# Optimization experiments

Hardware: AMD Instinct MI355X
Metric: run time of the kernel (lower is better)

## Reference

```python
import jax, jax.numpy as jnp
import numpy as np

B, C, H, W = 2, 256, 64, 64
NUM_HEADS = 4
DIM_HEAD_QK = 64
DIM_HEAD_V = 64  # dim_out // num_heads
DIM_OUT_QK = NUM_HEADS * DIM_HEAD_QK  # 256
DIM_OUT_V = NUM_HEADS * DIM_HEAD_V    # 256
SCALE = DIM_HEAD_QK ** -0.5


def rel_logits_1d(q, rel_k, permute):
    # q: (Bh, Hq, Wq, d), rel_k: (2*Wq-1, d)
    Bh, Hq, Wq, d = q.shape
    R = 2 * Wq - 1
    x = jnp.einsum('bhwd,rd->bhwr', q, rel_k)              # (Bh, Hq, Wq, R)
    x = x.reshape(-1, Wq, R)
    x_pad = jnp.pad(x, ((0, 0), (0, 0), (0, 1))).reshape(x.shape[0], -1)
    x_pad = jnp.pad(x_pad, ((0, 0), (0, Wq - 1)))
    x_pad = x_pad.reshape(-1, Wq + 1, R)
    x = x_pad[:, :Wq, Wq - 1:]                              # (Bh*Hq, Wq, Wq)
    x = x.reshape(Bh, Hq, 1, Wq, Wq)
    x = jnp.broadcast_to(x, (Bh, Hq, Hq, Wq, Wq))
    return jnp.transpose(x, permute)


def pos_embed_rel(q, height_rel, width_rel):
    # q: (Bh, HW, d)
    Bh = q.shape[0]
    qr = q.reshape(Bh, H, W, -1)
    rel_w = rel_logits_1d(qr, width_rel, (0, 1, 3, 2, 4))   # (Bh, H, W, H, W)
    qt = jnp.transpose(qr, (0, 2, 1, 3))                    # (Bh, W, H, d)
    rel_h = rel_logits_1d(qt, height_rel, (0, 3, 1, 4, 2))  # (Bh, H, W, H, W)
    return (rel_h + rel_w).reshape(Bh, H * W, H * W)


def setup_inputs() -> dict:
    key = jax.random.key(0)
    k1, k2, k3, k4 = jax.random.split(key, 4)
    x = jax.random.normal(k1, (B, C, H, W), dtype=jnp.float32)
    qkv_w = jax.random.normal(k2, (2 * DIM_OUT_QK + DIM_OUT_V, C), dtype=jnp.float32) * (C ** -0.5)
    height_rel = jax.random.normal(k3, (2 * H - 1, DIM_HEAD_QK), dtype=jnp.float32) * SCALE
    width_rel = jax.random.normal(k4, (2 * W - 1, DIM_HEAD_QK), dtype=jnp.float32) * SCALE
    return {"x": x, "qkv_w": qkv_w, "height_rel": height_rel, "width_rel": width_rel}


def reference(x, qkv_w, height_rel, width_rel):
    # 1x1 conv == channel matmul
    qkv = jnp.einsum('bchw,oc->bohw', x, qkv_w)             # (B, 768, H, W)
    q, k, v = jnp.split(qkv, [DIM_OUT_QK, 2 * DIM_OUT_QK], axis=1)
    HW = H * W
    q = q.reshape(B * NUM_HEADS, DIM_HEAD_QK, HW).transpose(0, 2, 1)  # (Bh, HW, d)
    k = k.reshape(B * NUM_HEADS, DIM_HEAD_QK, HW)                     # (Bh, d, HW)
    v = v.reshape(B * NUM_HEADS, DIM_HEAD_V, HW).transpose(0, 2, 1)   # (Bh, HW, dv)
    attn = jnp.einsum('bnd,bdm->bnm', q, k) * SCALE + pos_embed_rel(q, height_rel, width_rel)
    attn = jax.nn.softmax(attn, axis=-1)
    out = jnp.einsum('bnm,bmd->bnd', attn, v)               # (Bh, HW, dv)
    out = out.transpose(0, 2, 1).reshape(B, DIM_OUT_V, H, W)
    return out
```

## Files before the change

kernel.cpp:

```cpp
#include <hip/hip_runtime.h>
#include <hip/hip_bf16.h>

typedef __attribute__((ext_vector_type(8))) short bf16x8;
typedef __attribute__((ext_vector_type(4))) float f32x4;

static __device__ __forceinline__ f32x4 mfma16(bf16x8 a, bf16x8 b, f32x4 c) {
    return __builtin_amdgcn_mfma_f32_16x16x32_bf16(a, b, c, 0, 0, 0);
}
static __device__ __forceinline__ void gll16(const void* g, void* l) {
    __builtin_amdgcn_global_load_lds(
        (const __attribute__((address_space(1))) unsigned int*)g,
        (__attribute__((address_space(3))) unsigned int*)l, 16, 0, 0);
}

#define LOG2E 1.44269504f

__global__ __launch_bounds__(256, 4) void qkv_kernel(
    const float* __restrict__ x, const float* __restrict__ w,
    __hip_bfloat16* __restrict__ qb, __hip_bfloat16* __restrict__ kb,
    __hip_bfloat16* __restrict__ vt)
{
    alignas(16) __shared__ __hip_bfloat16 sA[64 * 72];
    alignas(16) __shared__ __hip_bfloat16 sB[64 * 72];
    const int nb = blockIdx.x * 64;
    const int ob = blockIdx.y * 64;
    const int b  = blockIdx.z;
    const int tid  = threadIdx.x;
    const int lane = tid & 63;
    const int wv   = tid >> 6;
    const int quad = lane >> 4;
    const int l16  = lane & 15;

    f32x4 acc[4];
    for (int i = 0; i < 4; i++) acc[i] = (f32x4)0.f;

    for (int k0 = 0; k0 < 256; k0 += 64) {
        __syncthreads();
        {
            const int o = tid >> 2, c0 = (tid & 3) << 4;
            const float* srcw = w + (ob + o) * 256 + k0 + c0;
            union { bf16x8 v; __hip_bfloat16 h[8]; } u0, u1;
            #pragma unroll
            for (int i = 0; i < 2; i++) {
                float4 f = *(const float4*)(srcw + i * 4);
                u0.h[4*i+0] = __float2bfloat16(f.x); u0.h[4*i+1] = __float2bfloat16(f.y);
                u0.h[4*i+2] = __float2bfloat16(f.z); u0.h[4*i+3] = __float2bfloat16(f.w);
            }
            #pragma unroll
            for (int i = 0; i < 2; i++) {
                float4 f = *(const float4*)(srcw + 8 + i * 4);
                u1.h[4*i+0] = __float2bfloat16(f.x); u1.h[4*i+1] = __float2bfloat16(f.y);
                u1.h[4*i+2] = __float2bfloat16(f.z); u1.h[4*i+3] = __float2bfloat16(f.w);
            }
            *(bf16x8*)&sA[o * 72 + c0]     = u0.v;
            *(bf16x8*)&sA[o * 72 + c0 + 8] = u1.v;
        }
        {
            const int c = tid >> 2, n0 = (tid & 3) << 4;
            const int csw = c ^ ((tid & 3) * 16);
            const float* srcx = x + ((size_t)b * 256 + k0 + c) * 4096 + nb + n0;
            #pragma unroll
            for (int i = 0; i < 4; i++) {
                float4 f = *(const float4*)(srcx + i * 4);
                sB[(n0 + 4*i + 0) * 72 + csw] = __float2bfloat16(f.x);
                sB[(n0 + 4*i + 1) * 72 + csw] = __float2bfloat16(f.y);
                sB[(n0 + 4*i + 2) * 72 + csw] = __float2bfloat16(f.z);
                sB[(n0 + 4*i + 3) * 72 + csw] = __float2bfloat16(f.w);
            }
        }
        __syncthreads();
        const __hip_bfloat16* aRow = &sA[(16 * wv + l16) * 72];
        #pragma unroll
        for (int ks = 0; ks < 2; ks++) {
            bf16x8 af = *(const bf16x8*)&aRow[ks * 32 + quad * 8];
            #pragma unroll
            for (int ct = 0; ct < 4; ct++) {
                bf16x8 bfv = *(const bf16x8*)&sB[(16 * ct + l16) * 72
                                                 + ((ks * 32 + quad * 8) ^ (ct * 16))];
                acc[ct] = mfma16(af, bfv, acc[ct]);
            }
        }
    }
    if (ob < 512) {
        __syncthreads();
        #pragma unroll
        for (int ct = 0; ct < 4; ct++) {
            union { short4 s; __hip_bfloat16 hh[4]; } u;
            #pragma unroll
            for (int r = 0; r < 4; r++) u.hh[r] = __float2bfloat16(acc[ct][r]);
            *(short4*)&sA[(16 * ct + l16) * 72 + 16 * wv + 4 * quad] = u.s;
        }
        __syncthreads();
        const int n_l = tid >> 2, d16 = (tid & 3) * 16;
        const int n = nb + n_l;
        const __hip_bfloat16* srcl = &sA[n_l * 72 + d16];
        bf16x8 v0 = *(const bf16x8*)srcl;
        bf16x8 v1 = *(const bf16x8*)(srcl + 8);
        const int bhh = b * 4 + ((ob & 255) >> 6);
        if (ob < 256) {
            __hip_bfloat16* dst = qb + ((size_t)bhh * 4096 + n) * 64;
            *(bf16x8*)(dst + d16)     = v0;
            *(bf16x8*)(dst + d16 + 8) = v1;
        } else {
            const int s = (n & 7) << 3;
            __hip_bfloat16* dst = kb + ((size_t)bhh * 4096 + n) * 64;
            *(bf16x8*)(dst + (d16 ^ s))       = v0;
            *(bf16x8*)(dst + ((d16 + 8) ^ s)) = v1;
        }
    } else {
        __syncthreads();
        #pragma unroll
        for (int ct = 0; ct < 4; ct++)
            #pragma unroll
            for (int r = 0; r < 4; r++)
                sA[(16 * wv + quad * 4 + r) * 72 + 16 * ct + l16] = __float2bfloat16(acc[ct][r]);
        int o2 = (ob - 512) + 16 * wv + l16;
        int bhh = b * 4 + (o2 >> 6), d = o2 & 63;
        const __hip_bfloat16* srcl = &sA[(16 * wv + l16) * 72 + 16 * quad];
        __hip_bfloat16* vrow = vt + ((size_t)bhh * 64 + d) * 4096;
        const int kt = quad & 1;
        const int gbase = nb + (quad >> 1) * 32;
        const int dsw = (d & 7) << 3;
        #pragma unroll
        for (int m = 0; m < 4; m++) {
            short4 val = *(const short4*)(srcl + 4 * m);
            int P4 = gbase + 8 * m + 4 * kt;
            *(short4*)(vrow + (P4 ^ dsw)) = val;
        }
    }
}

__global__ __launch_bounds__(512, 4) void attn_kernel(
    const __hip_bfloat16* __restrict__ qb, const __hip_bfloat16* __restrict__ kb,
    const __hip_bfloat16* __restrict__ vt, const float* __restrict__ hrel,
    const float* __restrict__ wrel, float* __restrict__ out)
{
    extern __shared__ __align__(16) char smem[];
    alignas(16) __shared__ __hip_bfloat16 sRH[64 * 66];

    const int h    = blockIdx.x;
    const int bh   = blockIdx.y;
    const int tid  = threadIdx.x;
    const int lane = tid & 63;
    const int wv   = tid >> 6;
    const int qg   = wv >> 2;
    const int kg   = wv & 3;
    const int quad = lane >> 4;
    const int l16  = lane & 15;

    __hip_bfloat16* sQ   = (__hip_bfloat16*)smem;
    __hip_bfloat16* sW   = (__hip_bfloat16*)smem + 64 * 72;
    __hip_bfloat16* sHRs = (__hip_bfloat16*)smem + 192 * 72;
    __hip_bfloat16* sRWt = (__hip_bfloat16*)smem;

    {
        int r = tid >> 3, d8 = (tid & 7) * 8;
        *(bf16x8*)&sQ[r * 72 + d8] =
            *(const bf16x8*)&qb[(((size_t)bh * 4096 + h * 64 + r)) * 64 + d8];
    }
    {
        int r = tid >> 2, c0 = (tid & 3) << 4;
        union { bf16x8 v; __hip_bfloat16 h8[8]; } u0, u1;
        #pragma unroll
        for (int i = 0; i < 2; i++) {
            float4 f = (r < 127) ? *(const float4*)&wrel[r * 64 + c0 + 4*i] : float4{0,0,0,0};
            u0.h8[4*i+0] = __float2bfloat16(f.x); u0.h8[4*i+1] = __float2bfloat16(f.y);
            u0.h8[4*i+2] = __float2bfloat16(f.z); u0.h8[4*i+3] = __float2bfloat16(f.w);
        }
        #pragma unroll
        for (int i = 0; i < 2; i++) {
            float4 f = (r < 127) ? *(const float4*)&wrel[r * 64 + c0 + 8 + 4*i] : float4{0,0,0,0};
            u1.h8[4*i+0] = __float2bfloat16(f.x); u1.h8[4*i+1] = __float2bfloat16(f.y);
            u1.h8[4*i+2] = __float2bfloat16(f.z); u1.h8[4*i+3] = __float2bfloat16(f.w);
        }
        *(bf16x8*)&sW[r * 72 + c0]     = u0.v;
        *(bf16x8*)&sW[r * 72 + c0 + 8] = u1.v;
    }
    {
        int r = tid >> 3, c0 = (tid & 7) * 8;
        union { bf16x8 v; __hip_bfloat16 h8[8]; } u0;
        #pragma unroll
        for (int i = 0; i < 2; i++) {
            float4 f = *(const float4*)&hrel[(63 - h + r) * 64 + c0 + 4*i];
            u0.h8[4*i+0] = __float2bfloat16(f.x); u0.h8[4*i+1] = __float2bfloat16(f.y);
            u0.h8[4*i+2] = __float2bfloat16(f.z); u0.h8[4*i+3] = __float2bfloat16(f.w);
        }
        *(bf16x8*)&sHRs[r * 72 + c0] = u0.v;
    }
    __syncthreads();

    const int g    = wv & 3;
    const int half = wv >> 2;
    const __hip_bfloat16* aRow = &sQ[(16 * g + l16) * 72];
    bf16x8 qf0 = *(const bf16x8*)&aRow[quad * 8];
    bf16x8 qf1 = *(const bf16x8*)&aRow[32 + quad * 8];
    bf16x8 qm[2][2];
    #pragma unroll
    for (int qt = 0; qt < 2; qt++) {
        const __hip_bfloat16* qr = &sQ[(qg * 32 + 16 * qt + l16) * 72];
        qm[qt][0] = *(const bf16x8*)&qr[quad * 8];
        qm[qt][1] = *(const bf16x8*)&qr[32 + quad * 8];
    }
    __syncthreads();

    {
        const int rbase = half * 64;
        #pragma unroll
        for (int ct = 0; ct < 4; ct++) {
            int rr = rbase + 16 * ct + l16;
            f32x4 a = (f32x4)0.f;
            a = mfma16(qf0, *(const bf16x8*)&sW[rr * 72 + quad * 8], a);
            a = mfma16(qf1, *(const bf16x8*)&sW[rr * 72 + 32 + quad * 8], a);
            #pragma unroll
            for (int r = 0; r < 4; r++) {
                int ww = 16 * g + quad * 4 + r;
                int wp = rr + ww - 63;
                if (wp >= 0 && wp < 64) sRWt[ww * 68 + wp] = __float2bfloat16(a[r]);
            }
        }
    }
    if (half == 0) {
        #pragma unroll
        for (int ct = 0; ct < 4; ct++) {
            f32x4 a = (f32x4)0.f;
            a = mfma16(qf0, *(const bf16x8*)&sHRs[(16 * ct + l16) * 72 + quad * 8], a);
            a = mfma16(qf1, *(const bf16x8*)&sHRs[(16 * ct + l16) * 72 + 32 + quad * 8], a);
            #pragma unroll
            for (int r = 0; r < 4; r++)
                sRH[(16 * g + quad * 4 + r) * 66 + 16 * ct + l16] = __float2bfloat16(a[r]);
        }
    }
    __syncthreads();

    union S4 { short4 s; __hip_bfloat16 h[4]; };
    float rwf[2][2][4];
    #pragma unroll
    for (int qt = 0; qt < 2; qt++)
        #pragma unroll
        for (int kt = 0; kt < 2; kt++) {
            S4 t;
            t.s = *(const short4*)&sRWt[(qg * 32 + 16 * qt + l16) * 68
                                        + 32 * (kg & 1) + 16 * kt + 4 * quad];
            #pragma unroll
            for (int r = 0; r < 4; r++)
                rwf[qt][kt][r] = LOG2E * __bfloat162float(t.h[r]);
        }
    __syncthreads();

    const char* kT = (const char*)kb + (size_t)bh * 524288 + wv * 1024 + lane * 16;
    const char* vT = (const char*)vt + (size_t)bh * 524288
                     + (size_t)(wv * 4 + quad) * 8192 + l16 * 16;

    gll16(kT,           smem + wv * 1024);
    gll16(kT + 8192,    smem + 8192 + wv * 1024);
    gll16(vT,           smem + 16384 + wv * 1024);
    gll16(vT + 262144,  smem + 24576 + wv * 1024);
    __syncthreads();

    f32x4 oacc[2][4];
    #pragma unroll
    for (int qt = 0; qt < 2; qt++)
        #pragma unroll
        for (int dt = 0; dt < 4; dt++) oacc[qt][dt] = (f32x4)0.f;
    f32x4 lacc[2] = {(f32x4)0.f, (f32x4)0.f};
    const bf16x8 vones = (bf16x8)(short)0x3F80;

    const int krowOff = (kg * 32 + l16) * 128;
    const int sw  = (l16 & 7) << 4;
    const int kA  = (quad * 16) ^ sw;
    const int kB  = (64 + quad * 16) ^ sw;
    const int vOff = 16384 + l16 * 256 + ((kg * 64 + quad * 16) ^ sw);

    const __hip_bfloat16* rh0 = &sRH[(qg * 32 + l16) * 66];
    const __hip_bfloat16* rh1 = &sRH[(qg * 32 + 16 + l16) * 66];
    const float SC = 0.125f * LOG2E;

    for (int j = 0; j < 32; j++) {
        const char* buf = smem + (j & 1) * 32768;
        if (j < 31) {
            char* nbuf = smem + ((j + 1) & 1) * 32768;
            const char* gk = kT + (size_t)(j + 1) * 16384;
            gll16(gk,          nbuf + wv * 1024);
            gll16(gk + 8192,   nbuf + 8192 + wv * 1024);
            const char* gv = vT + (size_t)(j + 1) * 256;
            gll16(gv,          nbuf + 16384 + wv * 1024);
            gll16(gv + 262144, nbuf + 24576 + wv * 1024);
        }

        const char* kr = buf + krowOff;
        bf16x8 kf00 = *(const bf16x8*)(kr + kA);
        bf16x8 kf01 = *(const bf16x8*)(kr + kB);
        bf16x8 kf10 = *(const bf16x8*)(kr + 2048 + kA);
        bf16x8 kf11 = *(const bf16x8*)(kr + 2048 + kB);

        f32x4 s[2][2];
        __builtin_amdgcn_s_setprio(1);
        #pragma unroll
        for (int qt = 0; qt < 2; qt++) {
            f32x4 a0 = (f32x4)0.f, a1 = (f32x4)0.f;
            a0 = mfma16(kf00, qm[qt][0], a0);
            a0 = mfma16(kf01, qm[qt][1], a0);
            a1 = mfma16(kf10, qm[qt][0], a1);
            a1 = mfma16(kf11, qm[qt][1], a1);
            s[qt][0] = a0; s[qt][1] = a1;
        }
        __builtin_amdgcn_s_setprio(0);

        const int hp = 2 * j + (kg >> 1);
        bf16x8 pa[2];
        #pragma unroll
        for (int qt = 0; qt < 2; qt++) {
            float rhb = LOG2E * __bfloat162float((qt ? rh1 : rh0)[hp]);
            float pv[8];
            #pragma unroll
            for (int r = 0; r < 4; r++)
                pv[r] = __builtin_amdgcn_exp2f(fmaf(s[qt][0][r], SC, rwf[qt][0][r] + rhb));
            #pragma unroll
            for (int r = 0; r < 4; r++)
                pv[4 + r] = __builtin_amdgcn_exp2f(fmaf(s[qt][1][r], SC, rwf[qt][1][r] + rhb));
            union { bf16x8 v; __hip_bfloat162 b2[4]; } pu;
            #pragma unroll
            for (int pi = 0; pi < 4; pi++)
                pu.b2[pi] = __float22bfloat162_rn(float2{pv[2 * pi], pv[2 * pi + 1]});
            pa[qt] = pu.v;
        }

        __builtin_amdgcn_s_setprio(1);
        #pragma unroll
        for (int dt = 0; dt < 4; dt++) {
            bf16x8 vf = *(const bf16x8*)(buf + vOff + dt * 4096);
            oacc[0][dt] = mfma16(pa[0], vf, oacc[0][dt]);
            oacc[1][dt] = mfma16(pa[1], vf, oacc[1][dt]);
        }
        lacc[0] = mfma16(pa[0], vones, lacc[0]);
        lacc[1] = mfma16(pa[1], vones, lacc[1]);
        __builtin_amdgcn_s_setprio(0);
        __syncthreads();
    }

    float* obuf = (float*)smem;
    if (kg != 0) {
        float* rb = obuf + (kg - 1) * 4672;
        #pragma unroll
        for (int qt = 0; qt < 2; qt++)
            #pragma unroll
            for (int dt = 0; dt < 4; dt++)
                *(f32x4*)&rb[qg * 2304 + (16 * dt + l16) * 36 + 16 * qt + 4 * quad]
                    = oacc[qt][dt];
        if (l16 == 0)
            #pragma unroll
            for (int qt = 0; qt < 2; qt++)
                #pragma unroll
                for (int r = 0; r < 4; r++)
                    rb[4608 + qg * 32 + 16 * qt + 4 * quad + r] = lacc[qt][r];
    }
    __syncthreads();
    if (kg == 0) {
        #pragma unroll
        for (int rg = 0; rg < 3; rg++) {
            const float* rb = obuf + rg * 4672;
            #pragma unroll
            for (int qt = 0; qt < 2; qt++) {
                #pragma unroll
                for (int dt = 0; dt < 4; dt++)
                    oacc[qt][dt] += *(const f32x4*)&rb[qg * 2304 + (16 * dt + l16) * 36
                                                       + 16 * qt + 4 * quad];
                #pragma unroll
                for (int r = 0; r < 4; r++)
                    lacc[qt][r] += rb[4608 + qg * 32 + 16 * qt + 4 * quad + r];
            }
        }
        const int b = bh >> 2, head = bh & 3;
        #pragma unroll
        for (int qt = 0; qt < 2; qt++) {
            f32x4 lv;
            #pragma unroll
            for (int r = 0; r < 4; r++) lv[r] = 1.f / lacc[qt][r];
            #pragma unroll
            for (int dt = 0; dt < 4; dt++) {
                f32x4 o = oacc[qt][dt] * lv;
                int dv = 16 * dt + l16;
                int q0 = qg * 32 + 16 * qt + 4 * quad;
                *(f32x4*)&out[((size_t)(b * 256 + head * 64 + dv)) * 4096 + h * 64 + q0] = o;
            }
        }
    }
}

extern "C" void kernel_launch(void* const* d_in, const int* in_sizes, int n_in,
                              void* d_out, int out_size, void* d_ws, size_t ws_size,
                              hipStream_t stream) {
    const float* x     = (const float*)d_in[0];
    const float* qkv_w = (const float*)d_in[1];
    const float* hrel  = (const float*)d_in[2];
    const float* wrel  = (const float*)d_in[3];
    float* out = (float*)d_out;

    __hip_bfloat16* qb = (__hip_bfloat16*)d_ws;
    __hip_bfloat16* kb = qb + (size_t)8 * 4096 * 64;
    __hip_bfloat16* vt = kb + (size_t)8 * 4096 * 64;

    qkv_kernel<<<dim3(64, 12, 2), 256, 0, stream>>>(x, qkv_w, qb, kb, vt);
    attn_kernel<<<dim3(64, 8), 512, 65536, stream>>>(qb, kb, vt, hrel, wrel, out);
}
```

Before: 125.4 us.

## Prefetch QKV projection tiles into registers and deepen attention K/V pipeline

In the QKV projection kernel, the next k-slice of weights and inputs is now loaded into registers while the current slice is being multiplied, so global load latency overlaps the MFMAs. In the attention kernel, K/V tiles are issued two iterations ahead into the double buffer. Partial vmcnt waits plus raw s_barrier replace the full __syncthreads, so one tile's loads stay in flight while the other is consumed. This adds register pressure in the projection kernel. It also relies on correct manual waitcnt counting, and the LDS-direct loads must not race with the barriers.

```diff
diff --git a/kernel.cpp b/kernel.cpp
--- a/kernel.cpp
+++ b/kernel.cpp
@@ -34,41 +34,56 @@
     f32x4 acc[4];
     for (int i = 0; i < 4; i++) acc[i] = (f32x4)0.f;
 
-    for (int k0 = 0; k0 < 256; k0 += 64) {
+    const int oA = tid >> 2, cA = (tid & 3) << 4;
+    const float* srcw = w + (ob + oA) * 256 + cA;
+    const int cB = tid >> 2, nB = (tid & 3) << 4;
+    const int csw = cB ^ ((tid & 3) * 16);
+    const float* srcx = x + ((size_t)b * 256 + cB) * 4096 + nb + nB;
+
+    float4 ra[4], rb4[4];
+    #pragma unroll
+    for (int i = 0; i < 4; i++) ra[i]  = *(const float4*)(srcw + i * 4);
+    #pragma unroll
+    for (int i = 0; i < 4; i++) rb4[i] = *(const float4*)(srcx + i * 4);
+
+    for (int t = 0; t < 4; t++) {
         __syncthreads();
         {
-            const int o = tid >> 2, c0 = (tid & 3) << 4;
-            const float* srcw = w + (ob + o) * 256 + k0 + c0;
             union { bf16x8 v; __hip_bfloat16 h[8]; } u0, u1;
             #pragma unroll
             for (int i = 0; i < 2; i++) {
-                float4 f = *(const float4*)(srcw + i * 4);
+                float4 f = ra[i];
                 u0.h[4*i+0] = __float2bfloat16(f.x); u0.h[4*i+1] = __float2bfloat16(f.y);
                 u0.h[4*i+2] = __float2bfloat16(f.z); u0.h[4*i+3] = __float2bfloat16(f.w);
             }
             #pragma unroll
             for (int i = 0; i < 2; i++) {
-                float4 f = *(const float4*)(srcw + 8 + i * 4);
+                float4 f = ra[2 + i];
                 u1.h[4*i+0] = __float2bfloat16(f.x); u1.h[4*i+1] = __float2bfloat16(f.y);
                 u1.h[4*i+2] = __float2bfloat16(f.z); u1.h[4*i+3] = __float2bfloat16(f.w);
             }
-            *(bf16x8*)&sA[o * 72 + c0]     = u0.v;
-            *(bf16x8*)&sA[o * 72 + c0 + 8] = u1.v;
+            *(bf16x8*)&sA[oA * 72 + cA]     = u0.v;
+            *(bf16x8*)&sA[oA * 72 + cA + 8] = u1.v;
         }
         {
-            const int c = tid >> 2, n0 = (tid & 3) << 4;
-            const int csw = c ^ ((tid & 3) * 16);
-            const float* srcx = x + ((size_t)b * 256 + k0 + c) * 4096 + nb + n0;
             #pragma unroll
             for (int i = 0; i < 4; i++) {
-                float4 f = *(const float4*)(srcx + i * 4);
-                sB[(n0 + 4*i + 0) * 72 + csw] = __float2bfloat16(f.x);
-                sB[(n0 + 4*i + 1) * 72 + csw] = __float2bfloat16(f.y);
-                sB[(n0 + 4*i + 2) * 72 + csw] = __float2bfloat16(f.z);
-                sB[(n0 + 4*i + 3) * 72 + csw] = __float2bfloat16(f.w);
+                float4 f = rb4[i];
+                sB[(nB + 4*i + 0) * 72 + csw] = __float2bfloat16(f.x);
+                sB[(nB + 4*i + 1) * 72 + csw] = __float2bfloat16(f.y);
+                sB[(nB + 4*i + 2) * 72 + csw] = __float2bfloat16(f.z);
+                sB[(nB + 4*i + 3) * 72 + csw] = __float2bfloat16(f.w);
             }
         }
         __syncthreads();
+        if (t < 3) {
+            #pragma unroll
+            for (int i = 0; i < 4; i++)
+                ra[i]  = *(const float4*)(srcw + (t + 1) * 64 + i * 4);
+            #pragma unroll
+            for (int i = 0; i < 4; i++)
+                rb4[i] = *(const float4*)(srcx + (size_t)(t + 1) * 64 * 4096 + i * 4);
+        }
         const __hip_bfloat16* aRow = &sA[(16 * wv + l16) * 72];
         #pragma unroll
         for (int ks = 0; ks < 2; ks++) {
@@ -251,11 +266,14 @@
     const char* vT = (const char*)vt + (size_t)bh * 524288
                      + (size_t)(wv * 4 + quad) * 8192 + l16 * 16;
 
-    gll16(kT,           smem + wv * 1024);
-    gll16(kT + 8192,    smem + 8192 + wv * 1024);
-    gll16(vT,           smem + 16384 + wv * 1024);
-    gll16(vT + 262144,  smem + 24576 + wv * 1024);
-    __syncthreads();
+    gll16(kT,                smem + wv * 1024);
+    gll16(kT + 8192,         smem + 8192 + wv * 1024);
+    gll16(vT,                smem + 16384 + wv * 1024);
+    gll16(vT + 262144,       smem + 24576 + wv * 1024);
+    gll16(kT + 16384,        smem + 32768 + wv * 1024);
+    gll16(kT + 16384 + 8192, smem + 32768 + 8192 + wv * 1024);
+    gll16(vT + 256,          smem + 32768 + 16384 + wv * 1024);
+    gll16(vT + 262144 + 256, smem + 32768 + 24576 + wv * 1024);
 
     f32x4 oacc[2][4];
     #pragma unroll
@@ -277,15 +295,10 @@
 
     for (int j = 0; j < 32; j++) {
         const char* buf = smem + (j & 1) * 32768;
-        if (j < 31) {
-            char* nbuf = smem + ((j + 1) & 1) * 32768;
-            const char* gk = kT + (size_t)(j + 1) * 16384;
-            gll16(gk,          nbuf + wv * 1024);
-            gll16(gk + 8192,   nbuf + 8192 + wv * 1024);
-            const char* gv = vT + (size_t)(j + 1) * 256;
-            gll16(gv,          nbuf + 16384 + wv * 1024);
-            gll16(gv + 262144, nbuf + 24576 + wv * 1024);
-        }
+        if (j < 31) asm volatile("s_waitcnt vmcnt(4)" ::: "memory");
+        else        asm volatile("s_waitcnt vmcnt(0)" ::: "memory");
+        __builtin_amdgcn_s_barrier();
+        __builtin_amdgcn_sched_barrier(0);
 
         const char* kr = buf + krowOff;
         bf16x8 kf00 = *(const bf16x8*)(kr + kA);
@@ -335,7 +348,18 @@
         lacc[0] = mfma16(pa[0], vones, lacc[0]);
         lacc[1] = mfma16(pa[1], vones, lacc[1]);
         __builtin_amdgcn_s_setprio(0);
-        __syncthreads();
+
+        __builtin_amdgcn_sched_barrier(0);
+        __builtin_amdgcn_s_barrier();
+        if (j < 30) {
+            char* nb2 = smem + (j & 1) * 32768;
+            const char* gk = kT + (size_t)(j + 2) * 16384;
+            gll16(gk,          nb2 + wv * 1024);
+            gll16(gk + 8192,   nb2 + 8192 + wv * 1024);
+            const char* gv = vT + (size_t)(j + 2) * 256;
+            gll16(gv,          nb2 + 16384 + wv * 1024);
+            gll16(gv + 262144, nb2 + 24576 + wv * 1024);
+        }
     }
 
     float* obuf = (float*)smem;
```

Result: no change. 127.8 us (+1.9%).

## Pre-transpose x to bf16 and double-buffer QKV projection with async LDS loads

Applied to the files above, without the earlier changes.

Adds a prep kernel that converts x to bf16 in a swizzled position-major layout, staged through the output buffer as scratch. The QKV GEMM then streams x tiles into LDS with global_load_lds and double-buffers them. Each wave keeps its weight fragments in registers rather than staging them through shared memory. This removes the per-block redundant fp32 conversion and strided transposed LDS stores. The cost is an extra kernel launch and an extra pass over x through global memory.

```diff
diff --git a/kernel.cpp b/kernel.cpp
--- a/kernel.cpp
+++ b/kernel.cpp
@@ -12,16 +12,57 @@
         (const __attribute__((address_space(1))) unsigned int*)g,
         (__attribute__((address_space(3))) unsigned int*)l, 16, 0, 0);
 }
+static __device__ __forceinline__ bf16x8 pack8(float4 a, float4 b) {
+    union { bf16x8 v; __hip_bfloat162 h[4]; } u;
+    u.h[0] = __float22bfloat162_rn(float2{a.x, a.y});
+    u.h[1] = __float22bfloat162_rn(float2{a.z, a.w});
+    u.h[2] = __float22bfloat162_rn(float2{b.x, b.y});
+    u.h[3] = __float22bfloat162_rn(float2{b.z, b.w});
+    return u.v;
+}
 
 #define LOG2E 1.44269504f
 
+__global__ __launch_bounds__(256, 8) void prep_kernel(
+    const float* __restrict__ x, __hip_bfloat16* __restrict__ xt)
+{
+    alignas(16) __shared__ __hip_bfloat16 sT[64 * 72];
+    const int bx = blockIdx.x;
+    const int by = blockIdx.y;
+    const int b  = blockIdx.z;
+    const int tid = threadIdx.x;
+
+    const int cp = tid >> 3;
+    const int n8 = (tid & 7) * 8;
+    const float* s0 = x + ((size_t)b * 256 + by * 64 + 2 * cp) * 4096 + bx * 64 + n8;
+    float4 f0 = *(const float4*)(s0);
+    float4 f1 = *(const float4*)(s0 + 4);
+    float4 g0 = *(const float4*)(s0 + 4096);
+    float4 g1 = *(const float4*)(s0 + 4096 + 4);
+    float c0v[8] = {f0.x, f0.y, f0.z, f0.w, f1.x, f1.y, f1.z, f1.w};
+    float c1v[8] = {g0.x, g0.y, g0.z, g0.w, g1.x, g1.y, g1.z, g1.w};
+    #pragma unroll
+    for (int i = 0; i < 8; i++) {
+        __hip_bfloat162 p = __float22bfloat162_rn(float2{c0v[i], c1v[i]});
+        *(__hip_bfloat162*)&sT[(n8 + i) * 72 + 2 * cp] = p;
+    }
+    __syncthreads();
+
+    const int n = tid >> 2, c16 = (tid & 3) * 16;
+    bf16x8 v0 = *(const bf16x8*)&sT[n * 72 + c16];
+    bf16x8 v1 = *(const bf16x8*)&sT[n * 72 + c16 + 8];
+    const int s = (n & 7) << 3;
+    __hip_bfloat16* dst = xt + ((size_t)b * 4096 + bx * 64 + n) * 256 + by * 64;
+    *(bf16x8*)(dst + (c16 ^ s))       = v0;
+    *(bf16x8*)(dst + ((c16 + 8) ^ s)) = v1;
+}
+
 __global__ __launch_bounds__(256, 4) void qkv_kernel(
-    const float* __restrict__ x, const float* __restrict__ w,
+    const float* __restrict__ w, const __hip_bfloat16* __restrict__ xt,
     __hip_bfloat16* __restrict__ qb, __hip_bfloat16* __restrict__ kb,
     __hip_bfloat16* __restrict__ vt)
 {
-    alignas(16) __shared__ __hip_bfloat16 sA[64 * 72];
-    alignas(16) __shared__ __hip_bfloat16 sB[64 * 72];
+    extern __shared__ __align__(16) char smem[];
     const int nb = blockIdx.x * 64;
     const int ob = blockIdx.y * 64;
     const int b  = blockIdx.z;
@@ -31,69 +72,63 @@
     const int quad = lane >> 4;
     const int l16  = lane & 15;
 
+    const char* xbase = (const char*)xt
+        + ((size_t)b * 4096 + nb + 16 * wv + (lane >> 3)) * 512 + (lane & 7) * 16;
+
+    gll16(xbase,        smem + wv * 2048);
+    gll16(xbase + 4096, smem + wv * 2048 + 1024);
+
+    bf16x8 af[4][2];
+    {
+        const float* wrow = w + (ob + 16 * wv + l16) * 256 + quad * 8;
+        #pragma unroll
+        for (int t = 0; t < 4; t++)
+            #pragma unroll
+            for (int ks = 0; ks < 2; ks++) {
+                const float* p = wrow + t * 64 + ks * 32;
+                af[t][ks] = pack8(*(const float4*)p, *(const float4*)(p + 4));
+            }
+    }
     f32x4 acc[4];
+    #pragma unroll
     for (int i = 0; i < 4; i++) acc[i] = (f32x4)0.f;
 
-    for (int k0 = 0; k0 < 256; k0 += 64) {
+    __syncthreads();
+
+    const int swB = (l16 & 7) << 4;
+    #pragma unroll
+    for (int t = 0; t < 4; t++) {
+        if (t < 3) {
+            char* nbuf = smem + ((t + 1) & 1) * 8192;
+            gll16(xbase + (t + 1) * 128,        nbuf + wv * 2048);
+            gll16(xbase + (t + 1) * 128 + 4096, nbuf + wv * 2048 + 1024);
+        }
+        const char* buf = smem + (t & 1) * 8192;
+        #pragma unroll
+        for (int ks = 0; ks < 2; ks++) {
+            #pragma unroll
+            for (int ct = 0; ct < 4; ct++) {
+                bf16x8 bfv = *(const bf16x8*)(buf + (16 * ct + l16) * 128
+                                              + ((ks * 64 + quad * 16) ^ swB));
+                acc[ct] = mfma16(af[t][ks], bfv, acc[ct]);
+            }
+        }
         __syncthreads();
-        {
-            const int o = tid >> 2, c0 = (tid & 3) << 4;
-            const float* srcw = w + (ob + o) * 256 + k0 + c0;
-            union { bf16x8 v; __hip_bfloat16 h[8]; } u0, u1;
-            #pragma unroll
-            for (int i = 0; i < 2; i++) {
-                float4 f = *(const float4*)(srcw + i * 4);
-                u0.h[4*i+0] = __float2bfloat16(f.x); u0.h[4*i+1] = __float2bfloat16(f.y);
-                u0.h[4*i+2] = __float2bfloat16(f.z); u0.h[4*i+3] = __float2bfloat16(f.w);
-            }
-            #pragma unroll
-            for (int i = 0; i < 2; i++) {
-                float4 f = *(const float4*)(srcw + 8 + i * 4);
-                u1.h[4*i+0] = __float2bfloat16(f.x); u1.h[4*i+1] = __float2bfloat16(f.y);
-                u1.h[4*i+2] = __float2bfloat16(f.z); u1.h[4*i+3] = __float2bfloat16(f.w);
-            }
-            *(bf16x8*)&sA[o * 72 + c0]     = u0.v;
-            *(bf16x8*)&sA[o * 72 + c0 + 8] = u1.v;
-        }
-        {
-            const int c = tid >> 2, n0 = (tid & 3) << 4;
-            const int csw = c ^ ((tid & 3) * 16);
-            const float* srcx = x + ((size_t)b * 256 + k0 + c) * 4096 + nb + n0;
-            #pragma unroll
-            for (int i = 0; i < 4; i++) {
-                float4 f = *(const float4*)(srcx + i * 4);
-                sB[(n0 + 4*i + 0) * 72 + csw] = __float2bfloat16(f.x);
-                sB[(n0 + 4*i + 1) * 72 + csw] = __float2bfloat16(f.y);
-                sB[(n0 + 4*i + 2) * 72 + csw] = __float2bfloat16(f.z);
-                sB[(n0 + 4*i + 3) * 72 + csw] = __float2bfloat16(f.w);
-            }
-        }
-        __syncthreads();
-        const __hip_bfloat16* aRow = &sA[(16 * wv + l16) * 72];
-        #pragma unroll
-        for (int ks = 0; ks < 2; ks++) {
-            bf16x8 af = *(const bf16x8*)&aRow[ks * 32 + quad * 8];
-            #pragma unroll
-            for (int ct = 0; ct < 4; ct++) {
-                bf16x8 bfv = *(const bf16x8*)&sB[(16 * ct + l16) * 72
-                                                 + ((ks * 32 + quad * 8) ^ (ct * 16))];
-                acc[ct] = mfma16(af, bfv, acc[ct]);
-            }
-        }
-    }
+    }
+
+    __hip_bfloat16* eA = (__hip_bfloat16*)smem;
     if (ob < 512) {
-        __syncthreads();
         #pragma unroll
         for (int ct = 0; ct < 4; ct++) {
             union { short4 s; __hip_bfloat16 hh[4]; } u;
             #pragma unroll
             for (int r = 0; r < 4; r++) u.hh[r] = __float2bfloat16(acc[ct][r]);
-            *(short4*)&sA[(16 * ct + l16) * 72 + 16 * wv + 4 * quad] = u.s;
+            *(short4*)&eA[(16 * ct + l16) * 72 + 16 * wv + 4 * quad] = u.s;
         }
         __syncthreads();
         const int n_l = tid >> 2, d16 = (tid & 3) * 16;
         const int n = nb + n_l;
-        const __hip_bfloat16* srcl = &sA[n_l * 72 + d16];
+        const __hip_bfloat16* srcl = &eA[n_l * 72 + d16];
         bf16x8 v0 = *(const bf16x8*)srcl;
         bf16x8 v1 = *(const bf16x8*)(srcl + 8);
         const int bhh = b * 4 + ((ob & 255) >> 6);
@@ -108,15 +143,14 @@
             *(bf16x8*)(dst + ((d16 + 8) ^ s)) = v1;
         }
     } else {
-        __syncthreads();
         #pragma unroll
         for (int ct = 0; ct < 4; ct++)
             #pragma unroll
             for (int r = 0; r < 4; r++)
-                sA[(16 * wv + quad * 4 + r) * 72 + 16 * ct + l16] = __float2bfloat16(acc[ct][r]);
+                eA[(16 * wv + quad * 4 + r) * 72 + 16 * ct + l16] = __float2bfloat16(acc[ct][r]);
         int o2 = (ob - 512) + 16 * wv + l16;
         int bhh = b * 4 + (o2 >> 6), d = o2 & 63;
-        const __hip_bfloat16* srcl = &sA[(16 * wv + l16) * 72 + 16 * quad];
+        const __hip_bfloat16* srcl = &eA[(16 * wv + l16) * 72 + 16 * quad];
         __hip_bfloat16* vrow = vt + ((size_t)bhh * 64 + d) * 4096;
         const int kt = quad & 1;
         const int gbase = nb + (quad >> 1) * 32;
@@ -399,7 +433,9 @@
     __hip_bfloat16* qb = (__hip_bfloat16*)d_ws;
     __hip_bfloat16* kb = qb + (size_t)8 * 4096 * 64;
     __hip_bfloat16* vt = kb + (size_t)8 * 4096 * 64;
-
-    qkv_kernel<<<dim3(64, 12, 2), 256, 0, stream>>>(x, qkv_w, qb, kb, vt);
+    __hip_bfloat16* xt = (__hip_bfloat16*)d_out;
+
+    prep_kernel<<<dim3(64, 4, 2), 256, 0, stream>>>(x, xt);
+    qkv_kernel<<<dim3(64, 12, 2), 256, 16384, stream>>>(qkv_w, xt, qb, kb, vt);
     attn_kernel<<<dim3(64, 8), 512, 65536, stream>>>(qb, kb, vt, hrel, wrel, out);
 }
```

New measurement: 132.5 us. 1.06x slower.
